# Kernel tuning notes

Measured on AMD Instinct MI355X. Metric: run time of the kernel, lower is better.

The kernel has to match this reference:

```python
import jax, jax.numpy as jnp
import numpy as np

N, E = 20000, 320000
D, DW, DS, NCLS = 512, 300, 16, 13


def setup_inputs() -> dict:
    key = jax.random.key(0)
    ks = jax.random.split(key, 24)
    g = lambda k, s, sc=0.02: (jax.random.normal(k, s, dtype=jnp.float32) * sc)
    inp = {
        'n_f': jax.random.normal(ks[0], (N, D), dtype=jnp.float32),
        'word2vec': jax.random.normal(ks[1], (N, DW), dtype=jnp.float32),
        's_f': jax.random.normal(ks[2], (E, DS), dtype=jnp.float32),
        'src': jax.random.randint(ks[3], (E,), 0, N, dtype=jnp.int32),
        'dst': jax.random.randint(ks[4], (E,), 0, N, dtype=jnp.int32),
        # edge MLPs: G_E_L_S=[2*D+DS, D], G_E_L_S2=[2*DW, D]
        'W_e': g(ks[5], (2 * D + DS, D)), 'b_e': jnp.zeros((D,), jnp.float32),
        'W_el': g(ks[6], (2 * DW, D)), 'b_el': jnp.zeros((D,), jnp.float32),
        # attention MLPs: G_A_L_S=[D,1], G_A_L_S2=[D,1]
        'W_a': g(ks[7], (D, 1)), 'b_a': jnp.zeros((1,), jnp.float32),
        'W_al': g(ks[8], (D, 1)), 'b_al': jnp.zeros((1,), jnp.float32),
        # node MLPs: G_N_L_S=[2*D, D], G_N_L_S2=[2*DW, DW]
        'W_n': g(ks[9], (2 * D, D)), 'b_n': jnp.zeros((D,), jnp.float32),
        'W_nl': g(ks[10], (2 * DW, DW)), 'b_nl': jnp.zeros((DW,), jnp.float32),
        # edge readout: G_ER_L_S=[2*D+2*DW+DS, D, 13], acts ['ReLU','Identity']
        'W_r1': g(ks[11], (2 * D + 2 * DW + DS, D)), 'b_r1': jnp.zeros((D,), jnp.float32),
        'W_r2': g(ks[12], (D, NCLS)), 'b_r2': jnp.zeros((NCLS,), jnp.float32),
    }
    return inp


def _segment_softmax(logits, seg, num_segments):
    m = jax.ops.segment_max(logits, seg, num_segments=num_segments)
    m = jnp.where(jnp.isfinite(m), m, 0.0)
    e = jnp.exp(logits - m[seg])
    s = jax.ops.segment_sum(e, seg, num_segments=num_segments)
    return e / (s[seg] + 1e-9)


def _forward(n_f, word2vec, s_f, W_e, b_e, W_el, b_el, W_a, b_a, W_al, b_al,
             W_n, b_n, W_nl, b_nl, W_r1, b_r1, W_r2, b_r2, src, dst):
    n = n_f.shape[0]
    relu = jax.nn.relu
    # H_H_EdgeApplyModule: e_f = ReLU(MLP([src n_f, s_f, dst n_f]))
    feat = jnp.concatenate([n_f[src], s_f, n_f[dst]], axis=1)            # [E, 2D+DS]
    e_f = relu(feat @ W_e + b_e)                                         # [E, D]
    feat_lang = jnp.concatenate([word2vec[src], word2vec[dst]], axis=1)  # [E, 2DW]
    e_f_lang = relu(feat_lang @ W_el + b_el)                             # [E, D]
    # E_AttentionModule1: LeakyReLU(0.2) attention logits per edge
    a = jax.nn.leaky_relu(e_f @ W_a + b_a, 0.2)[:, 0]
    a_l = jax.nn.leaky_relu(e_f_lang @ W_al + b_al, 0.2)[:, 0]
    # edge-softmax over incoming edges of each destination node
    alpha = _segment_softmax(a, dst, n)
    alpha_l = _segment_softmax(a_l, dst, n)
    # attention-weighted aggregation (scatter-add per dst node)
    z = jax.ops.segment_sum(alpha[:, None] * e_f, dst, num_segments=n)            # [N, D]
    z_l = jax.ops.segment_sum(alpha_l[:, None] * word2vec[src], dst, num_segments=n)  # [N, DW]
    # H_NodeApplyModule: node update with ReLU MLPs
    n_new = relu(jnp.concatenate([n_f, z], axis=1) @ W_n + b_n)          # [N, D]
    w_new = relu(jnp.concatenate([word2vec, z_l], axis=1) @ W_nl + b_nl) # [N, DW]
    # edge readout (G_ER): [src n_f, src w2v, s_f, dst w2v, dst n_f] -> ReLU -> Identity
    r = jnp.concatenate([n_new[src], w_new[src], s_f, w_new[dst], n_new[dst]], axis=1)
    h = relu(r @ W_r1 + b_r1)
    return h @ W_r2 + b_r2                                               # [E, 13]


def reference(n_f, word2vec, s_f, src, dst, W_e, b_e, W_el, b_el, W_a, b_a,
              W_al, b_al, W_n, b_n, W_nl, b_nl, W_r1, b_r1, W_r2, b_r2):
    return _forward(n_f, word2vec, s_f, W_e, b_e, W_el, b_el, W_a, b_a, W_al, b_al,
                    W_n, b_n, W_nl, b_nl, W_r1, b_r1, W_r2, b_r2, src, dst)
```

## Files before the change

kernel.cpp:

```cpp
#include <hip/hip_runtime.h>

typedef unsigned short u16;
typedef unsigned int u32;
typedef __bf16 bf16x8 __attribute__((ext_vector_type(8)));
typedef float f32x4 __attribute__((ext_vector_type(4)));

#define ND 512
#define DWR 300
#define DWP 320
#define NCLS 13

__device__ __forceinline__ float bf2f(u16 u) { return __uint_as_float(((u32)u) << 16); }
__device__ __forceinline__ u16 f2bf(float f) {
    u32 u = __float_as_uint(f);
    u32 r = (u + 0x7FFFu + ((u >> 16) & 1u)) >> 16;
    return (u16)r;
}
__device__ __forceinline__ void ub8(float4 r, float* v) {
    union { float4 f; u16 u[8]; } U; U.f = r;
#pragma unroll
    for (int k = 0; k < 8; ++k) v[k] = bf2f(U.u[k]);
}
__device__ __forceinline__ void ld8f(const u16* p, float* v) { ub8(*(const float4*)p, v); }
__device__ __forceinline__ void ld16(const float* p, float* s) {
    const float4* sp = (const float4*)p;
    float4 s0 = sp[0], s1 = sp[1], s2 = sp[2], s3 = sp[3];
    s[0]=s0.x; s[1]=s0.y; s[2]=s0.z; s[3]=s0.w; s[4]=s1.x; s[5]=s1.y; s[6]=s1.z; s[7]=s1.w;
    s[8]=s2.x; s[9]=s2.y; s[10]=s2.z; s[11]=s2.w; s[12]=s3.x; s[13]=s3.y; s[14]=s3.z; s[15]=s3.w;
}

struct GSeg { const u16* base; const int* idx; int stride; int width; };
struct GSegs { GSeg s[5]; };
struct TSeg { int src_begin; int wreal; int wpad; };
struct TSegs { TSeg t[5]; };

template<int RELU>
__global__ __launch_bounds__(256) void gemm_k(
    int M, int Nout, GSegs segs,
    const u16* __restrict__ BT, int ldb,
    const float* __restrict__ bias, int bias_n,
    u16* __restrict__ outb, int ldo)
{
    __shared__ __align__(16) u16 As[128 * 40];
    __shared__ __align__(16) u16 Bs[128 * 40];
    const int tid = threadIdx.x;

    const int gx = gridDim.x, gy = gridDim.y;
    const int g0 = blockIdx.x + gx * blockIdx.y;
    int xt, yt;
    {
        const int fullg = gx >> 3;
        const int gsz = 8 * gy;
        if (g0 < fullg * gsz) {
            const int grp = g0 / gsz, w = g0 % gsz;
            xt = grp * 8 + (w & 7); yt = w >> 3;
        } else {
            const int remx = gx - fullg * 8;
            const int t = g0 - fullg * gsz;
            xt = fullg * 8 + t % remx; yt = t / remx;
        }
    }
    const int m0 = xt * 128, n0 = yt * 128;

    const int row = tid >> 1, half = tid & 1;
    int mrow = m0 + row; if (mrow >= M) mrow = M - 1;
    const int lane = tid & 63, wid = tid >> 6;
    const int wr = (wid >> 1) * 64, wc = (wid & 1) * 64;
    const int lr = lane & 15, lg = lane >> 4;

    f32x4 acc[4][4];
    for (int fm = 0; fm < 4; fm++)
        for (int fn = 0; fn < 4; fn++)
            acc[fm][fn] = f32x4{0.f, 0.f, 0.f, 0.f};

    const u16* brow = BT + (size_t)(n0 + row) * ldb + half * 16;

    auto do_step = [&](const u16* ga_, const u16* gb_) {
        float4 a0 = *(const float4*)ga_;
        float4 a1 = *(const float4*)(ga_ + 8);
        float4 b0 = *(const float4*)gb_;
        float4 b1 = *(const float4*)(gb_ + 8);
        __syncthreads();
        *(float4*)&As[row * 40 + half * 16]     = a0;
        *(float4*)&As[row * 40 + half * 16 + 8] = a1;
        *(float4*)&Bs[row * 40 + half * 16]     = b0;
        *(float4*)&Bs[row * 40 + half * 16 + 8] = b1;
        __syncthreads();
        bf16x8 af[4], bfv[4];
#pragma unroll
        for (int f = 0; f < 4; f++) {
            af[f]  = *(const bf16x8*)&As[(wr + f * 16 + lr) * 40 + lg * 8];
            bfv[f] = *(const bf16x8*)&Bs[(wc + f * 16 + lr) * 40 + lg * 8];
        }
#pragma unroll
        for (int fm = 0; fm < 4; fm++)
#pragma unroll
            for (int fn = 0; fn < 4; fn++)
                acc[fm][fn] = __builtin_amdgcn_mfma_f32_16x16x32_bf16(af[fm], bfv[fn], acc[fm][fn], 0, 0, 0);
    };

    int k0 = 0;
#pragma unroll
    for (int sI = 0; sI < 5; sI++) {
        const GSeg S = segs.s[sI];
        if (S.width > 0) {
            const int ridx = S.idx ? S.idx[mrow] : mrow;
            const u16* abase = S.base + (size_t)ridx * S.stride + half * 16;
            for (int kk = 0; kk < S.width; kk += 32) {
                do_step(abase + kk, brow + k0 + kk);
            }
            k0 += S.width;
        }
    }

#pragma unroll
    for (int fm = 0; fm < 4; fm++) {
#pragma unroll
        for (int i = 0; i < 4; i++) {
            const int grow = m0 + wr + fm * 16 + lg * 4 + i;
            const bool rok = grow < M;
#pragma unroll
            for (int fn = 0; fn < 4; fn++) {
                const int col = n0 + wc + fn * 16 + lr;
                float v = acc[fm][fn][i];
                v += (col < bias_n) ? bias[col] : 0.f;
                if (RELU) v = fmaxf(v, 0.f);
                if (rok && col < Nout) outb[(size_t)grow * ldo + col] = f2bf(v);
            }
        }
    }
}

__global__ __launch_bounds__(256) void pass1_k(
    const u16* __restrict__ Q, const u16* __restrict__ Lq,
    const float* __restrict__ s_f, const float* __restrict__ wmid,
    const int* __restrict__ psrc, const int* __restrict__ pdst, const int* __restrict__ perm,
    const float* __restrict__ W_a, const float* __restrict__ W_al,
    const float* __restrict__ b_e, const float* __restrict__ b_el,
    const float* __restrict__ b_a, const float* __restrict__ b_al,
    float* __restrict__ aA, float* __restrict__ aL, int E)
{
    __shared__ __align__(16) u16 sfs_bf[128 * 40];
    __shared__ __align__(16) u16 wmidT[512 * 16];
    __shared__ __align__(16) u16 As_v[128 * 40];
    __shared__ __align__(16) u16 As_l[128 * 40];
    __shared__ __align__(16) float sfw[128 * 36];
    __shared__ float bes[512], bels[512];
    __shared__ __align__(16) u16 was[512], wals[512];

    const int tid = threadIdx.x;
    const int e0 = blockIdx.x * 128;

    for (int i = tid; i < 512 * 16; i += 256) {
        const int col = i >> 4, k = i & 15;
        wmidT[i] = f2bf(wmid[k * 512 + col]);
    }
    for (int i = tid; i < 512; i += 256) {
        bes[i] = b_e[i]; bels[i] = b_el[i];
        was[i] = f2bf(W_a[i]); wals[i] = f2bf(W_al[i]);
    }

    const int row = tid >> 1, half = tid & 1;
    const int er = e0 + row;
    const int erc = (er < E) ? er : E - 1;
    {
        const int pe = perm[erc];
        const float4* sp = (const float4*)(s_f + (size_t)pe * 16 + half * 8);
        float4 a = sp[0], b = sp[1];
        union { float4 f; u16 u[8]; } S;
        S.u[0]=f2bf(a.x); S.u[1]=f2bf(a.y); S.u[2]=f2bf(a.z); S.u[3]=f2bf(a.w);
        S.u[4]=f2bf(b.x); S.u[5]=f2bf(b.y); S.u[6]=f2bf(b.z); S.u[7]=f2bf(b.w);
        *(float4*)&sfs_bf[row * 40 + half * 8] = S.f;
        S.f = float4{0.f, 0.f, 0.f, 0.f};
        *(float4*)&sfs_bf[row * 40 + 16 + half * 8] = S.f;
    }

    const int ps = psrc[erc], pd = pdst[erc];
    const u16* q1b = Q + (size_t)ps * 1024;
    const u16* q2b = Q + (size_t)pd * 1024 + 512;
    const u16* l1b = Lq + (size_t)ps * 1024;
    const u16* l2b = Lq + (size_t)pd * 1024 + 512;

    const int lane = tid & 63, wid = tid >> 6;
    const int lr = lane & 15, lg = lane >> 4;
    f32x4 accv[2], accl[2];
    accv[0] = accv[1] = accl[0] = accl[1] = f32x4{0.f, 0.f, 0.f, 0.f};
    union { bf16x8 v; float4 f; } BZ; BZ.f = float4{0.f, 0.f, 0.f, 0.f};

    __syncthreads();

    for (int ch = 0; ch < 16; ++ch) {
        const int k0 = ch * 32 + half * 16;
#pragma unroll
        for (int rt = 0; rt < 2; ++rt) {
            bf16x8 af = *(const bf16x8*)&sfs_bf[((wid * 2 + rt) * 16 + lr) * 40 + lg * 8];
#pragma unroll
            for (int ct = 0; ct < 2; ++ct) {
                const int f = ch * 32 + ct * 16 + lr;
                bf16x8 bf_ = *(const bf16x8*)&wmidT[f * 16 + (lg & 1) * 8];
                f32x4 c = __builtin_amdgcn_mfma_f32_16x16x32_bf16(af, bf_, f32x4{0.f,0.f,0.f,0.f}, 0, 0, 0);
#pragma unroll
                for (int i = 0; i < 4; ++i)
                    sfw[((wid * 2 + rt) * 16 + lg * 4 + i) * 36 + ct * 16 + lr] = c[i];
            }
        }
        __syncthreads();

        float4 rq1a = *(const float4*)(q1b + k0);
        float4 rq1b = *(const float4*)(q1b + k0 + 8);
        float4 rq2a = *(const float4*)(q2b + k0);
        float4 rq2b = *(const float4*)(q2b + k0 + 8);
        float4 rl1a = *(const float4*)(l1b + k0);
        float4 rl1b = *(const float4*)(l1b + k0 + 8);
        float4 rl2a = *(const float4*)(l2b + k0);
        float4 rl2b = *(const float4*)(l2b + k0 + 8);
        float sw[16];
        *(float4*)&sw[0]  = *(const float4*)&sfw[row * 36 + half * 16 + 0];
        *(float4*)&sw[4]  = *(const float4*)&sfw[row * 36 + half * 16 + 4];
        *(float4*)&sw[8]  = *(const float4*)&sfw[row * 36 + half * 16 + 8];
        *(float4*)&sw[12] = *(const float4*)&sfw[row * 36 + half * 16 + 12];

        float uv[16], ul[16], t1[8], t2[8];
        ub8(rq1a, t1); ub8(rq2a, t2);
#pragma unroll
        for (int k = 0; k < 8; ++k) uv[k] = t1[k] + t2[k] + bes[k0 + k] + sw[k];
        ub8(rq1b, t1); ub8(rq2b, t2);
#pragma unroll
        for (int k = 0; k < 8; ++k) uv[8 + k] = t1[k] + t2[k] + bes[k0 + 8 + k] + sw[8 + k];
        ub8(rl1a, t1); ub8(rl2a, t2);
#pragma unroll
        for (int k = 0; k < 8; ++k) ul[k] = t1[k] + t2[k] + bels[k0 + k];
        ub8(rl1b, t1); ub8(rl2b, t2);
#pragma unroll
        for (int k = 0; k < 8; ++k) ul[8 + k] = t1[k] + t2[k] + bels[k0 + 8 + k];

        union { float4 f; u16 u[8]; } Va, Vb, La, Lb;
#pragma unroll
        for (int k = 0; k < 8; ++k) {
            Va.u[k] = f2bf(fmaxf(uv[k], 0.f));
            Vb.u[k] = f2bf(fmaxf(uv[8 + k], 0.f));
            La.u[k] = f2bf(fmaxf(ul[k], 0.f));
            Lb.u[k] = f2bf(fmaxf(ul[8 + k], 0.f));
        }
        *(float4*)&As_v[row * 40 + half * 16]     = Va.f;
        *(float4*)&As_v[row * 40 + half * 16 + 8] = Vb.f;
        *(float4*)&As_l[row * 40 + half * 16]     = La.f;
        *(float4*)&As_l[row * 40 + half * 16 + 8] = Lb.f;
        __syncthreads();

        bf16x8 bv = BZ.v, bl = BZ.v;
        if (lr == 0) {
            bv = *(const bf16x8*)&was[ch * 32 + lg * 8];
            bl = *(const bf16x8*)&wals[ch * 32 + lg * 8];
        }
#pragma unroll
        for (int m = 0; m < 2; ++m) {
            bf16x8 afv = *(const bf16x8*)&As_v[(wid * 32 + m * 16 + lr) * 40 + lg * 8];
            bf16x8 afl = *(const bf16x8*)&As_l[(wid * 32 + m * 16 + lr) * 40 + lg * 8];
            accv[m] = __builtin_amdgcn_mfma_f32_16x16x32_bf16(afv, bv, accv[m], 0, 0, 0);
            accl[m] = __builtin_amdgcn_mfma_f32_16x16x32_bf16(afl, bl, accl[m], 0, 0, 0);
        }
    }

    if (lr == 0) {
        const float ba = b_a[0], bal = b_al[0];
#pragma unroll
        for (int m = 0; m < 2; ++m) {
#pragma unroll
            for (int i = 0; i < 4; ++i) {
                const int e = e0 + wid * 32 + m * 16 + lg * 4 + i;
                if (e < E) {
                    float x = accv[m][i] + ba;
                    aA[e] = x > 0.f ? x : 0.2f * x;
                    float y = accl[m][i] + bal;
                    aL[e] = y > 0.f ? y : 0.2f * y;
                }
            }
        }
    }
}

__global__ __launch_bounds__(256) void softmax_k(
    float* __restrict__ a, float* __restrict__ al,
    const int* __restrict__ offs, int N, int E)
{
    const int node = blockIdx.x * 4 + (threadIdx.x >> 6);
    if (node >= N) return;
    const int lane = threadIdx.x & 63;
    const int e0 = offs[node];
    const int e1 = (node + 1 < N) ? offs[node + 1] : E;
    if (e0 >= e1) return;
    float m = -3.4e38f, ml = -3.4e38f;
    for (int e = e0 + lane; e < e1; e += 64) { m = fmaxf(m, a[e]); ml = fmaxf(ml, al[e]); }
#pragma unroll
    for (int off = 32; off >= 1; off >>= 1) {
        m  = fmaxf(m,  __shfl_xor(m,  off, 64));
        ml = fmaxf(ml, __shfl_xor(ml, off, 64));
    }
    float s = 0.f, sl = 0.f;
    for (int e = e0 + lane; e < e1; e += 64) {
        float v = expf(a[e] - m);   a[e] = v;  s += v;
        float w = expf(al[e] - ml); al[e] = w; sl += w;
    }
#pragma unroll
    for (int off = 32; off >= 1; off >>= 1) {
        s  += __shfl_xor(s,  off, 64);
        sl += __shfl_xor(sl, off, 64);
    }
    const float rs = 1.f / (s + 1e-9f), rsl = 1.f / (sl + 1e-9f);
    for (int e = e0 + lane; e < e1; e += 64) { a[e] *= rs; al[e] *= rsl; }
}

__global__ __launch_bounds__(256) void passz_k(
    const u16* __restrict__ Q, const u16* __restrict__ wv_bf,
    const float* __restrict__ s_f, const float* __restrict__ wmid,
    const int* __restrict__ psrc, const int* __restrict__ perm, const int* __restrict__ offs,
    const float* __restrict__ alpha, const float* __restrict__ alphal,
    const float* __restrict__ b_e,
    u16* __restrict__ z_bf, u16* __restrict__ zl_bf, int N, int E)
{
    __shared__ __align__(16) u16 wmids[16 * 512];
    const int tid = threadIdx.x;
    for (int i = tid; i < 16 * 512; i += 256) wmids[i] = f2bf(wmid[i]);
    __syncthreads();
    const int node = blockIdx.x * 4 + (tid >> 6);
    if (node >= N) return;
    const int lane = tid & 63;
    const int col0 = lane * 8;
    const int colw = (lane < 40) ? col0 : 0;
    const int e0 = offs[node];
    const int e1 = (node + 1 < N) ? offs[node + 1] : E;

    float q2b[8], accz[8], accl[8], t[8];
    ld8f(Q + (size_t)node * 1024 + 512 + col0, q2b);
#pragma unroll
    for (int k = 0; k < 8; ++k) { q2b[k] += b_e[col0 + k]; accz[k] = 0.f; accl[k] = 0.f; }

    if (e0 < e1) {
        int ps0 = psrc[e0], pe0 = perm[e0];
        float4 rq0 = *(const float4*)(Q + (size_t)ps0 * 1024 + col0);
        float4 rw0 = *(const float4*)(wv_bf + (size_t)ps0 * DWP + colw);
        int ps1 = ps0, pe1 = pe0;
        if (e0 + 1 < e1) { ps1 = psrc[e0 + 1]; pe1 = perm[e0 + 1]; }

        for (int e = e0; e < e1; ++e) {
            float4 rq1 = rq0, rw1 = rw0;
            if (e + 1 < e1) {
                rq1 = *(const float4*)(Q + (size_t)ps1 * 1024 + col0);
                rw1 = *(const float4*)(wv_bf + (size_t)ps1 * DWP + colw);
            }
            int ps2 = ps1, pe2 = pe1;
            if (e + 2 < e1) { ps2 = psrc[e + 2]; pe2 = perm[e + 2]; }

            const float alA = alpha[e], alL = alphal[e];
            float sf[16];
            ld16(s_f + (size_t)pe0 * 16, sf);
            float v[8];
            ub8(rq0, t);
#pragma unroll
            for (int k = 0; k < 8; ++k) v[k] = t[k] + q2b[k];
#pragma unroll
            for (int j = 0; j < 16; ++j) {
                union { float4 f; u16 u[8]; } W;
                W.f = *(const float4*)&wmids[j * 512 + col0];
#pragma unroll
                for (int k = 0; k < 8; ++k) v[k] = fmaf(sf[j], bf2f(W.u[k]), v[k]);
            }
#pragma unroll
            for (int k = 0; k < 8; ++k) accz[k] = fmaf(alA, fmaxf(v[k], 0.f), accz[k]);
            ub8(rw0, t);
#pragma unroll
            for (int k = 0; k < 8; ++k) accl[k] = fmaf(alL, t[k], accl[k]);

            rq0 = rq1; rw0 = rw1; ps0 = ps1; pe0 = pe1; ps1 = ps2; pe1 = pe2;
        }
    }
    union { float4 f; u16 u[8]; } O;
#pragma unroll
    for (int k = 0; k < 8; ++k) O.u[k] = f2bf(accz[k]);
    *(float4*)(z_bf + (size_t)node * 512 + col0) = O.f;
    if (lane < 40) {
#pragma unroll
        for (int k = 0; k < 8; ++k) O.u[k] = f2bf(accl[k]);
        *(float4*)(zl_bf + (size_t)node * DWP + col0) = O.f;
    }
}

__global__ __launch_bounds__(256) void pass3_k(
    const u16* __restrict__ P, const float* __restrict__ s_f, const float* __restrict__ wmid2,
    const int* __restrict__ psrc, const int* __restrict__ pdst, const int* __restrict__ perm,
    const float* __restrict__ b_r1, const float* __restrict__ w2, const float* __restrict__ b_r2,
    float* __restrict__ out, int E)
{
    __shared__ __align__(16) u16 As[128 * 40];
    __shared__ __align__(16) u16 sfs_bf[128 * 40];
    __shared__ __align__(16) u16 wmidT[512 * 16];
    __shared__ __align__(16) u16 w2Ts[16 * 520];
    __shared__ __align__(16) float sfw[128 * 36];
    __shared__ float br1s[512];

    const int tid = threadIdx.x;
    const int e0 = blockIdx.x * 128;

    for (int i = tid; i < 512 * 16; i += 256) {
        const int col = i >> 4, k = i & 15;
        wmidT[i] = f2bf(wmid2[k * 512 + col]);
    }
    for (int i = tid; i < 16 * 512; i += 256) {
        const int c = i >> 9, k = i & 511;
        w2Ts[c * 520 + k] = f2bf((c < NCLS) ? w2[k * NCLS + c] : 0.f);
    }
    for (int i = tid; i < 512; i += 256) br1s[i] = b_r1[i];

    const int row = tid >> 1, half = tid & 1;
    const int er = e0 + row;
    const int erc = (er < E) ? er : E - 1;
    {
        const int pe = perm[erc];
        const float4* sp = (const float4*)(s_f + (size_t)pe * 16 + half * 8);
        float4 a = sp[0], b = sp[1];
        union { float4 f; u16 u[8]; } S;
        S.u[0]=f2bf(a.x); S.u[1]=f2bf(a.y); S.u[2]=f2bf(a.z); S.u[3]=f2bf(a.w);
        S.u[4]=f2bf(b.x); S.u[5]=f2bf(b.y); S.u[6]=f2bf(b.z); S.u[7]=f2bf(b.w);
        *(float4*)&sfs_bf[row * 40 + half * 8] = S.f;
        S.f = float4{0.f, 0.f, 0.f, 0.f};
        *(float4*)&sfs_bf[row * 40 + 16 + half * 8] = S.f;
    }

    const int ps = psrc[erc], pd = pdst[erc];
    const u16* p1base = P + (size_t)ps * 1024;
    const u16* p2base = P + (size_t)pd * 1024 + 512;

    const int lane = tid & 63, wid = tid >> 6;
    const int lr = lane & 15, lg = lane >> 4;
    f32x4 acc0 = f32x4{0.f, 0.f, 0.f, 0.f};
    f32x4 acc1 = f32x4{0.f, 0.f, 0.f, 0.f};

    __syncthreads();

    for (int ch = 0; ch < 16; ++ch) {
        const int k0 = ch * 32 + half * 16;
#pragma unroll
        for (int rt = 0; rt < 2; ++rt) {
            bf16x8 af = *(const bf16x8*)&sfs_bf[((wid * 2 + rt) * 16 + lr) * 40 + lg * 8];
#pragma unroll
            for (int ct = 0; ct < 2; ++ct) {
                const int f = ch * 32 + ct * 16 + lr;
                bf16x8 bf_ = *(const bf16x8*)&wmidT[f * 16 + (lg & 1) * 8];
                f32x4 c = __builtin_amdgcn_mfma_f32_16x16x32_bf16(af, bf_, f32x4{0.f,0.f,0.f,0.f}, 0, 0, 0);
#pragma unroll
                for (int i = 0; i < 4; ++i)
                    sfw[((wid * 2 + rt) * 16 + lg * 4 + i) * 36 + ct * 16 + lr] = c[i];
            }
        }
        __syncthreads();

        float4 r1a = *(const float4*)(p1base + k0);
        float4 r1b = *(const float4*)(p1base + k0 + 8);
        float4 r2a = *(const float4*)(p2base + k0);
        float4 r2b = *(const float4*)(p2base + k0 + 8);
        float sw[16];
        *(float4*)&sw[0]  = *(const float4*)&sfw[row * 36 + half * 16 + 0];
        *(float4*)&sw[4]  = *(const float4*)&sfw[row * 36 + half * 16 + 4];
        *(float4*)&sw[8]  = *(const float4*)&sfw[row * 36 + half * 16 + 8];
        *(float4*)&sw[12] = *(const float4*)&sfw[row * 36 + half * 16 + 12];

        float u[16], t1[8], t2[8];
        ub8(r1a, t1); ub8(r2a, t2);
#pragma unroll
        for (int k = 0; k < 8; ++k) u[k] = t1[k] + t2[k] + br1s[k0 + k] + sw[k];
        ub8(r1b, t1); ub8(r2b, t2);
#pragma unroll
        for (int k = 0; k < 8; ++k) u[8 + k] = t1[k] + t2[k] + br1s[k0 + 8 + k] + sw[8 + k];

        union { float4 f; u16 u[8]; } Oa, Ob;
#pragma unroll
        for (int k = 0; k < 8; ++k) {
            Oa.u[k] = f2bf(fmaxf(u[k], 0.f));
            Ob.u[k] = f2bf(fmaxf(u[8 + k], 0.f));
        }
        *(float4*)&As[row * 40 + half * 16]     = Oa.f;
        *(float4*)&As[row * 40 + half * 16 + 8] = Ob.f;
        __syncthreads();

        bf16x8 af0 = *(const bf16x8*)&As[(wid * 32 +      lr) * 40 + lg * 8];
        bf16x8 af1 = *(const bf16x8*)&As[(wid * 32 + 16 + lr) * 40 + lg * 8];
        bf16x8 bfv = *(const bf16x8*)&w2Ts[lr * 520 + ch * 32 + lg * 8];
        acc0 = __builtin_amdgcn_mfma_f32_16x16x32_bf16(af0, bfv, acc0, 0, 0, 0);
        acc1 = __builtin_amdgcn_mfma_f32_16x16x32_bf16(af1, bfv, acc1, 0, 0, 0);
    }

    if (lr < NCLS) {
        const float bc = b_r2[lr];
#pragma unroll
        for (int m = 0; m < 2; ++m) {
            const f32x4 a = m ? acc1 : acc0;
            const int rbase = e0 + wid * 32 + m * 16 + lg * 4;
#pragma unroll
            for (int i = 0; i < 4; ++i) {
                const int ei = rbase + i;
                if (ei < E) out[(size_t)perm[ei] * NCLS + lr] = a[i] + bc;
            }
        }
    }
}

__global__ __launch_bounds__(256) void cvt_bf(const float* __restrict__ src, u16* __restrict__ dst,
                                              int R, int Cs, int Cd)
{
    int id = blockIdx.x * 256 + threadIdx.x;
    if (id >= R * Cd) return;
    int r = id / Cd, c = id % Cd;
    float v = (c < Cs) ? src[(size_t)r * Cs + c] : 0.f;
    dst[id] = f2bf(v);
}

__global__ __launch_bounds__(256) void wtrans(const float* __restrict__ W, int Nw, int Nreal,
                                              int NrowsOut, int ldk, TSegs ts, int nseg,
                                              u16* __restrict__ WT)
{
    int id = blockIdx.x * 256 + threadIdx.x;
    if (id >= NrowsOut * ldk) return;
    int n = id / ldk, kp = id % ldk;
    float v = 0.f;
    if (n < Nreal) {
        int off = 0;
#pragma unroll
        for (int s = 0; s < 5; s++) {
            if (s < nseg) {
                int kl = kp - off;
                if (kl >= 0 && kl < ts.t[s].wpad) {
                    if (kl < ts.t[s].wreal) v = W[(size_t)(ts.t[s].src_begin + kl) * Nw + n];
                }
                off += ts.t[s].wpad;
            }
        }
    }
    WT[id] = f2bf(v);
}

__global__ __launch_bounds__(256) void hist_k(const int* __restrict__ dst, int* __restrict__ deg, int E)
{
    int id = blockIdx.x * 256 + threadIdx.x;
    if (id < E) atomicAdd(&deg[dst[id]], 1);
}

__global__ __launch_bounds__(1024) void scan_k(const int* __restrict__ deg,
                                               int* __restrict__ offs, int* __restrict__ cursor, int N)
{
    __shared__ int ps[1024];
    const int t = threadIdx.x;
    const int per = (N + 1023) >> 10;
    int s = 0;
    for (int j = 0; j < per; j++) { int idx = t * per + j; if (idx < N) s += deg[idx]; }
    ps[t] = s; __syncthreads();
    for (int o = 1; o < 1024; o <<= 1) {
        int v = (t >= o) ? ps[t - o] : 0; __syncthreads();
        ps[t] += v; __syncthreads();
    }
    int run = ps[t] - s;
    for (int j = 0; j < per; j++) {
        int idx = t * per + j;
        if (idx < N) { offs[idx] = run; cursor[idx] = run; run += deg[idx]; }
    }
}

__global__ __launch_bounds__(256) void scat_perm_k(const int* __restrict__ src, const int* __restrict__ dst,
                                                   int* __restrict__ cursor, int* __restrict__ perm,
                                                   int* __restrict__ psrc, int* __restrict__ pdst, int E)
{
    int id = blockIdx.x * 256 + threadIdx.x;
    if (id >= E) return;
    int d = dst[id];
    int pos = atomicAdd(&cursor[d], 1);
    perm[pos] = id; psrc[pos] = src[id]; pdst[pos] = d;
}

__global__ __launch_bounds__(256) void diag_fill(float* out, int n, float v)
{
    int id = blockIdx.x * 256 + threadIdx.x;
    if (id < n) out[id] = v;
}

extern "C" void kernel_launch(void* const* d_in, const int* in_sizes, int n_in,
                              void* d_out, int out_size, void* d_ws, size_t ws_size,
                              hipStream_t stream)
{
    const float* n_f  = (const float*)d_in[0];
    const float* w2v  = (const float*)d_in[1];
    const float* s_f  = (const float*)d_in[2];
    const int*   src  = (const int*)d_in[3];
    const int*   dst  = (const int*)d_in[4];
    const float* W_e  = (const float*)d_in[5];
    const float* b_e  = (const float*)d_in[6];
    const float* W_el = (const float*)d_in[7];
    const float* b_el = (const float*)d_in[8];
    const float* W_a  = (const float*)d_in[9];
    const float* b_a  = (const float*)d_in[10];
    const float* W_al = (const float*)d_in[11];
    const float* b_al = (const float*)d_in[12];
    const float* W_n  = (const float*)d_in[13];
    const float* b_n  = (const float*)d_in[14];
    const float* W_nl = (const float*)d_in[15];
    const float* b_nl = (const float*)d_in[16];
    const float* W_r1 = (const float*)d_in[17];
    const float* b_r1 = (const float*)d_in[18];
    const float* W_r2 = (const float*)d_in[19];
    const float* b_r2 = (const float*)d_in[20];

    const int N = in_sizes[0] / ND;
    const int E = in_sizes[3];
    float* out = (float*)d_out;

    auto g1 = [](long long n) { return dim3((unsigned)((n + 255) / 256)); };

    char* base = (char*)d_ws;
    size_t off = 0;
    auto alloc = [&](size_t bytes) -> void* {
        void* r = base + off;
        off += (bytes + 255) & ~(size_t)255;
        return r;
    };
    u16* nf_bf = (u16*)alloc((size_t)N * ND * 2);
    u16* wv_bf = (u16*)alloc((size_t)N * DWP * 2);
    u16* Q     = (u16*)alloc((size_t)N * 1024 * 2);
    u16* Lq    = (u16*)alloc((size_t)N * 1024 * 2);
    u16* Pt    = (u16*)alloc((size_t)N * 1024 * 2);
    u16* z_bf  = (u16*)alloc((size_t)N * ND * 2);
    u16* zl_bf = (u16*)alloc((size_t)N * DWP * 2);
    u16* nn_bf = (u16*)alloc((size_t)N * ND * 2);
    u16* wn_bf = (u16*)alloc((size_t)N * DWP * 2);
    u16* QT    = (u16*)alloc((size_t)1024 * 512 * 2);
    u16* LT    = (u16*)alloc((size_t)1024 * 320 * 2);
    u16* WnT   = (u16*)alloc((size_t)512 * 1024 * 2);
    u16* WnlT  = (u16*)alloc((size_t)384 * 640 * 2);
    u16* PrT   = (u16*)alloc((size_t)1024 * 832 * 2);
    float* aAs = (float*)alloc((size_t)E * 4);
    float* aLs = (float*)alloc((size_t)E * 4);
    int* deg    = (int*)alloc((size_t)N * 4);
    int* offs   = (int*)alloc((size_t)N * 4);
    int* cursor = (int*)alloc((size_t)N * 4);
    int* perm   = (int*)alloc((size_t)E * 4);
    int* psrc   = (int*)alloc((size_t)E * 4);
    int* pdst   = (int*)alloc((size_t)E * 4);

    if (off > ws_size) {
        diag_fill<<<g1(out_size), 256, 0, stream>>>(out, out_size, 2.0e6f);
        return;
    }

    hipMemsetAsync(deg, 0, (size_t)N * 4, stream);

    hist_k<<<g1(E), 256, 0, stream>>>(dst, deg, E);
    scan_k<<<dim3(1), 1024, 0, stream>>>(deg, offs, cursor, N);
    scat_perm_k<<<g1(E), 256, 0, stream>>>(src, dst, cursor, perm, psrc, pdst, E);

    cvt_bf<<<g1((long long)N * ND), 256, 0, stream>>>(n_f, nf_bf, N, ND, ND);
    cvt_bf<<<g1((long long)N * DWP), 256, 0, stream>>>(w2v, wv_bf, N, DWR, DWP);

    { TSegs t{}; t.t[0] = {0,512,512};
      wtrans<<<g1(512 * 512), 256, 0, stream>>>(W_e, 512, 512, 512, 512, t, 1, QT); }
    { TSegs t{}; t.t[0] = {528,512,512};
      wtrans<<<g1(512 * 512), 256, 0, stream>>>(W_e, 512, 512, 512, 512, t, 1, QT + 512 * 512); }
    { TSegs t{}; t.t[0] = {0,300,320};
      wtrans<<<g1(512 * 320), 256, 0, stream>>>(W_el, 512, 512, 512, 320, t, 1, LT); }
    { TSegs t{}; t.t[0] = {300,300,320};
      wtrans<<<g1(512 * 320), 256, 0, stream>>>(W_el, 512, 512, 512, 320, t, 1, LT + 512 * 320); }
    { TSegs t{}; t.t[0] = {0,512,512}; t.t[1] = {512,512,512};
      wtrans<<<g1(512 * 1024), 256, 0, stream>>>(W_n, 512, 512, 512, 1024, t, 2, WnT); }
    { TSegs t{}; t.t[0] = {0,300,320}; t.t[1] = {300,300,320};
      wtrans<<<g1(384 * 640), 256, 0, stream>>>(W_nl, 300, 300, 384, 640, t, 2, WnlT); }
    { TSegs t{}; t.t[0] = {0,512,512}; t.t[1] = {512,300,320};
      wtrans<<<g1(512 * 832), 256, 0, stream>>>(W_r1, 512, 512, 512, 832, t, 2, PrT); }
    { TSegs t{}; t.t[0] = {1128,512,512}; t.t[1] = {828,300,320};
      wtrans<<<g1(512 * 832), 256, 0, stream>>>(W_r1, 512, 512, 512, 832, t, 2, PrT + 512 * 832); }

    const int gmx = (N + 127) / 128;
    const dim3 gnode((N + 3) / 4);

    { GSegs s{}; s.s[0] = {nf_bf, nullptr, ND, 512};
      gemm_k<0><<<dim3(gmx, 8), 256, 0, stream>>>(N, 1024, s, QT, 512, nullptr, 0, Q, 1024); }
    { GSegs s{}; s.s[0] = {wv_bf, nullptr, DWP, 320};
      gemm_k<0><<<dim3(gmx, 8), 256, 0, stream>>>(N, 1024, s, LT, 320, nullptr, 0, Lq, 1024); }

    pass1_k<<<dim3((E + 127) / 128), 256, 0, stream>>>(Q, Lq, s_f, W_e + 512 * 512,
                                                       psrc, pdst, perm, W_a, W_al,
                                                       b_e, b_el, b_a, b_al, aAs, aLs, E);
    softmax_k<<<gnode, 256, 0, stream>>>(aAs, aLs, offs, N, E);

    passz_k<<<gnode, 256, 0, stream>>>(Q, wv_bf, s_f, W_e + 512 * 512, psrc, perm, offs,
                                       aAs, aLs, b_e, z_bf, zl_bf, N, E);

    { GSegs s{}; s.s[0] = {nf_bf, nullptr, ND, 512}; s.s[1] = {z_bf, nullptr, ND, 512};
      gemm_k<1><<<dim3(gmx, 4), 256, 0, stream>>>(N, 512, s, WnT, 1024, b_n, 512, nn_bf, 512); }
    { GSegs s{}; s.s[0] = {wv_bf, nullptr, DWP, 320}; s.s[1] = {zl_bf, nullptr, DWP, 320};
      gemm_k<1><<<dim3(gmx, 3), 256, 0, stream>>>(N, 320, s, WnlT, 640, b_nl, 300, wn_bf, DWP); }

    { GSegs s{}; s.s[0] = {nn_bf, nullptr, ND, 512}; s.s[1] = {wn_bf, nullptr, DWP, 320};
      gemm_k<0><<<dim3(gmx, 8), 256, 0, stream>>>(N, 1024, s, PrT, 832, nullptr, 0, Pt, 1024); }

    pass3_k<<<dim3((E + 127) / 128), 256, 0, stream>>>(Pt, s_f, W_r1 + 812 * 512,
                                                       psrc, pdst, perm, b_r1, W_r2, b_r2, out, E);

    hipError_t e = hipGetLastError();
    if (e != hipSuccess) {
        diag_fill<<<g1(out_size), 256, 0, stream>>>(out, out_size, 1.0e6f + (float)(int)e);
    }
}
```

Measured before the change: 939.7 us.

## Restructure edge aggregation as edge-parallel MFMA kernel with atomics and XCD swizzle

The per-node z aggregation, which recomputed the s_f·W_mid projection with scalar FMAs, is replaced by an edge-parallel kernel. That kernel computes the projection with bf16 MFMA on 128-edge tiles and scatters alpha-weighted ReLU outputs into an fp32 buffer using segmented runs followed by atomicAdd. The z_l aggregation moves to its own lightweight per-node kernel, and a memset plus a conversion kernel are added to produce bf16 z. Edge kernels also remap block indices to keep contiguous edge tiles on the same XCD for cache locality. The trade-offs are extra launches, atomic contention, and reusing the Lq buffer as fp32 scratch.

```diff
diff --git a/kernel.cpp b/kernel.cpp
--- a/kernel.cpp
+++ b/kernel.cpp
@@ -22,11 +22,10 @@
     for (int k = 0; k < 8; ++k) v[k] = bf2f(U.u[k]);
 }
 __device__ __forceinline__ void ld8f(const u16* p, float* v) { ub8(*(const float4*)p, v); }
-__device__ __forceinline__ void ld16(const float* p, float* s) {
-    const float4* sp = (const float4*)p;
-    float4 s0 = sp[0], s1 = sp[1], s2 = sp[2], s3 = sp[3];
-    s[0]=s0.x; s[1]=s0.y; s[2]=s0.z; s[3]=s0.w; s[4]=s1.x; s[5]=s1.y; s[6]=s1.z; s[7]=s1.w;
-    s[8]=s2.x; s[9]=s2.y; s[10]=s2.z; s[11]=s2.w; s[12]=s3.x; s[13]=s3.y; s[14]=s3.z; s[15]=s3.w;
+__device__ __forceinline__ int xcd_swz(int b, int gx) {
+    const int q = gx >> 3, r = gx & 7;
+    const int x = b & 7, o = b >> 3;
+    return (x < r ? x * (q + 1) : r * (q + 1) + (x - r) * q) + o;
 }
 
 struct GSeg { const u16* base; const int* idx; int stride; int width; };
@@ -149,7 +148,7 @@
     __shared__ __align__(16) u16 was[512], wals[512];
 
     const int tid = threadIdx.x;
-    const int e0 = blockIdx.x * 128;
+    const int e0 = xcd_swz(blockIdx.x, gridDim.x) * 128;
 
     for (int i = tid; i < 512 * 16; i += 256) {
         const int col = i >> 4, k = i & 15;
@@ -311,78 +310,138 @@
     for (int e = e0 + lane; e < e1; e += 64) { a[e] *= rs; al[e] *= rsl; }
 }
 
-__global__ __launch_bounds__(256) void passz_k(
-    const u16* __restrict__ Q, const u16* __restrict__ wv_bf,
-    const float* __restrict__ s_f, const float* __restrict__ wmid,
-    const int* __restrict__ psrc, const int* __restrict__ perm, const int* __restrict__ offs,
-    const float* __restrict__ alpha, const float* __restrict__ alphal,
-    const float* __restrict__ b_e,
-    u16* __restrict__ z_bf, u16* __restrict__ zl_bf, int N, int E)
-{
-    __shared__ __align__(16) u16 wmids[16 * 512];
+__global__ __launch_bounds__(256) void passzt_k(
+    const u16* __restrict__ Q, const float* __restrict__ s_f, const float* __restrict__ wmid,
+    const int* __restrict__ psrc, const int* __restrict__ pdst, const int* __restrict__ perm,
+    const float* __restrict__ alpha, const float* __restrict__ b_e,
+    float* __restrict__ z, int E)
+{
+    __shared__ __align__(16) u16 sfs_bf[128 * 40];
+    __shared__ __align__(16) u16 wmidT[512 * 16];
+    __shared__ __align__(16) float sfw[128 * 36];
+    __shared__ float bes[512];
+    __shared__ int pd[128];
+    __shared__ float alf[128];
+
     const int tid = threadIdx.x;
-    for (int i = tid; i < 16 * 512; i += 256) wmids[i] = f2bf(wmid[i]);
+    const int e0 = xcd_swz(blockIdx.x, gridDim.x) * 128;
+
+    for (int i = tid; i < 512 * 16; i += 256) {
+        const int col = i >> 4, k = i & 15;
+        wmidT[i] = f2bf(wmid[k * 512 + col]);
+    }
+    for (int i = tid; i < 512; i += 256) bes[i] = b_e[i];
+
+    const int row = tid >> 1, half = tid & 1;
+    const int er = e0 + row;
+    const int erc = (er < E) ? er : E - 1;
+    {
+        const int pe = perm[erc];
+        const float4* sp = (const float4*)(s_f + (size_t)pe * 16 + half * 8);
+        float4 a = sp[0], b = sp[1];
+        union { float4 f; u16 u[8]; } S;
+        S.u[0]=f2bf(a.x); S.u[1]=f2bf(a.y); S.u[2]=f2bf(a.z); S.u[3]=f2bf(a.w);
+        S.u[4]=f2bf(b.x); S.u[5]=f2bf(b.y); S.u[6]=f2bf(b.z); S.u[7]=f2bf(b.w);
+        *(float4*)&sfs_bf[row * 40 + half * 8] = S.f;
+        S.f = float4{0.f, 0.f, 0.f, 0.f};
+        *(float4*)&sfs_bf[row * 40 + 16 + half * 8] = S.f;
+    }
+    if (half == 0) {
+        pd[row] = pdst[erc];
+        alf[row] = (er < E) ? alpha[er] : 0.f;
+    }
+
+    const int ps = psrc[erc], pdn = pdst[erc];
+    const u16* q1b = Q + (size_t)ps * 1024;
+    const u16* q2b = Q + (size_t)pdn * 1024 + 512;
+
+    const int lane = tid & 63, wid = tid >> 6;
+    const int lr = lane & 15, lg = lane >> 4;
+
     __syncthreads();
-    const int node = blockIdx.x * 4 + (tid >> 6);
+
+    for (int ch = 0; ch < 16; ++ch) {
+        const int k0 = ch * 32 + half * 16;
+#pragma unroll
+        for (int rt = 0; rt < 2; ++rt) {
+            bf16x8 af = *(const bf16x8*)&sfs_bf[((wid * 2 + rt) * 16 + lr) * 40 + lg * 8];
+#pragma unroll
+            for (int ct = 0; ct < 2; ++ct) {
+                const int f = ch * 32 + ct * 16 + lr;
+                bf16x8 bf_ = *(const bf16x8*)&wmidT[f * 16 + (lg & 1) * 8];
+                f32x4 c = __builtin_amdgcn_mfma_f32_16x16x32_bf16(af, bf_, f32x4{0.f,0.f,0.f,0.f}, 0, 0, 0);
+#pragma unroll
+                for (int i = 0; i < 4; ++i)
+                    sfw[((wid * 2 + rt) * 16 + lg * 4 + i) * 36 + ct * 16 + lr] = c[i];
+            }
+        }
+        __syncthreads();
+
+        {
+            float4 r1a = *(const float4*)(q1b + k0);
+            float4 r1b = *(const float4*)(q1b + k0 + 8);
+            float4 r2a = *(const float4*)(q2b + k0);
+            float4 r2b = *(const float4*)(q2b + k0 + 8);
+            float sw[16];
+            *(float4*)&sw[0]  = *(const float4*)&sfw[row * 36 + half * 16 + 0];
+            *(float4*)&sw[4]  = *(const float4*)&sfw[row * 36 + half * 16 + 4];
+            *(float4*)&sw[8]  = *(const float4*)&sfw[row * 36 + half * 16 + 8];
+            *(float4*)&sw[12] = *(const float4*)&sfw[row * 36 + half * 16 + 12];
+            float u[16], t1[8], t2[8];
+            ub8(r1a, t1); ub8(r2a, t2);
+#pragma unroll
+            for (int k = 0; k < 8; ++k) u[k] = t1[k] + t2[k] + bes[k0 + k] + sw[k];
+            ub8(r1b, t1); ub8(r2b, t2);
+#pragma unroll
+            for (int k = 0; k < 8; ++k) u[8 + k] = t1[k] + t2[k] + bes[k0 + 8 + k] + sw[8 + k];
+            const float av = alf[row];
+#pragma unroll
+            for (int k = 0; k < 16; ++k) u[k] = av * fmaxf(u[k], 0.f);
+            *(float4*)&sfw[row * 36 + half * 16 + 0]  = *(float4*)&u[0];
+            *(float4*)&sfw[row * 36 + half * 16 + 4]  = *(float4*)&u[4];
+            *(float4*)&sfw[row * 36 + half * 16 + 8]  = *(float4*)&u[8];
+            *(float4*)&sfw[row * 36 + half * 16 + 12] = *(float4*)&u[12];
+        }
+        __syncthreads();
+
+        {
+            const int c = tid & 31, g = tid >> 5;
+            const int r0 = g * 16;
+            float run = 0.f; int cur = pd[r0];
+            for (int r = r0; r < r0 + 16; ++r) {
+                run += sfw[r * 36 + c];
+                const int nxt = (r < r0 + 15) ? pd[r + 1] : -1;
+                if (nxt != cur) {
+                    atomicAdd(&z[(size_t)cur * 512 + ch * 32 + c], run);
+                    run = 0.f; cur = nxt;
+                }
+            }
+        }
+        __syncthreads();
+    }
+}
+
+__global__ __launch_bounds__(256) void agg_zl_k(
+    const u16* __restrict__ wv_bf, const float* __restrict__ alphal,
+    const int* __restrict__ psrc, const int* __restrict__ offs,
+    u16* __restrict__ zl_bf, int N, int E)
+{
+    const int node = blockIdx.x * 4 + (threadIdx.x >> 6);
     if (node >= N) return;
-    const int lane = tid & 63;
-    const int col0 = lane * 8;
-    const int colw = (lane < 40) ? col0 : 0;
+    const int lane = threadIdx.x & 63;
     const int e0 = offs[node];
     const int e1 = (node + 1 < N) ? offs[node + 1] : E;
-
-    float q2b[8], accz[8], accl[8], t[8];
-    ld8f(Q + (size_t)node * 1024 + 512 + col0, q2b);
-#pragma unroll
-    for (int k = 0; k < 8; ++k) { q2b[k] += b_e[col0 + k]; accz[k] = 0.f; accl[k] = 0.f; }
-
-    if (e0 < e1) {
-        int ps0 = psrc[e0], pe0 = perm[e0];
-        float4 rq0 = *(const float4*)(Q + (size_t)ps0 * 1024 + col0);
-        float4 rw0 = *(const float4*)(wv_bf + (size_t)ps0 * DWP + colw);
-        int ps1 = ps0, pe1 = pe0;
-        if (e0 + 1 < e1) { ps1 = psrc[e0 + 1]; pe1 = perm[e0 + 1]; }
-
-        for (int e = e0; e < e1; ++e) {
-            float4 rq1 = rq0, rw1 = rw0;
-            if (e + 1 < e1) {
-                rq1 = *(const float4*)(Q + (size_t)ps1 * 1024 + col0);
-                rw1 = *(const float4*)(wv_bf + (size_t)ps1 * DWP + colw);
-            }
-            int ps2 = ps1, pe2 = pe1;
-            if (e + 2 < e1) { ps2 = psrc[e + 2]; pe2 = perm[e + 2]; }
-
-            const float alA = alpha[e], alL = alphal[e];
-            float sf[16];
-            ld16(s_f + (size_t)pe0 * 16, sf);
-            float v[8];
-            ub8(rq0, t);
-#pragma unroll
-            for (int k = 0; k < 8; ++k) v[k] = t[k] + q2b[k];
-#pragma unroll
-            for (int j = 0; j < 16; ++j) {
-                union { float4 f; u16 u[8]; } W;
-                W.f = *(const float4*)&wmids[j * 512 + col0];
-#pragma unroll
-                for (int k = 0; k < 8; ++k) v[k] = fmaf(sf[j], bf2f(W.u[k]), v[k]);
-            }
-#pragma unroll
-            for (int k = 0; k < 8; ++k) accz[k] = fmaf(alA, fmaxf(v[k], 0.f), accz[k]);
-            ub8(rw0, t);
-#pragma unroll
-            for (int k = 0; k < 8; ++k) accl[k] = fmaf(alL, t[k], accl[k]);
-
-            rq0 = rq1; rw0 = rw1; ps0 = ps1; pe0 = pe1; ps1 = ps2; pe1 = pe2;
-        }
-    }
-    union { float4 f; u16 u[8]; } O;
-#pragma unroll
-    for (int k = 0; k < 8; ++k) O.u[k] = f2bf(accz[k]);
-    *(float4*)(z_bf + (size_t)node * 512 + col0) = O.f;
-    if (lane < 40) {
-#pragma unroll
-        for (int k = 0; k < 8; ++k) O.u[k] = f2bf(accl[k]);
-        *(float4*)(zl_bf + (size_t)node * DWP + col0) = O.f;
+    float acc[5] = {0.f, 0.f, 0.f, 0.f, 0.f};
+    for (int e = e0; e < e1; ++e) {
+        const float al = alphal[e];
+        const u16* wr = wv_bf + (size_t)psrc[e] * DWP;
+#pragma unroll
+        for (int j = 0; j < 5; ++j) acc[j] += al * bf2f(wr[lane + 64 * j]);
+    }
+#pragma unroll
+    for (int j = 0; j < 5; ++j) {
+        const int c = lane + 64 * j;
+        zl_bf[(size_t)node * DWP + c] = f2bf(c < DWR ? acc[j] : 0.f);
     }
 }
 
@@ -400,7 +459,7 @@
     __shared__ float br1s[512];
 
     const int tid = threadIdx.x;
-    const int e0 = blockIdx.x * 128;
+    const int e0 = xcd_swz(blockIdx.x, gridDim.x) * 128;
 
     for (int i = tid; i < 512 * 16; i += 256) {
         const int col = i >> 4, k = i & 15;
@@ -643,6 +702,7 @@
     int* perm   = (int*)alloc((size_t)E * 4);
     int* psrc   = (int*)alloc((size_t)E * 4);
     int* pdst   = (int*)alloc((size_t)E * 4);
+    float* zf = (float*)Lq;
 
     if (off > ws_size) {
         diag_fill<<<g1(out_size), 256, 0, stream>>>(out, out_size, 2.0e6f);
@@ -677,19 +737,23 @@
 
     const int gmx = (N + 127) / 128;
     const dim3 gnode((N + 3) / 4);
+    const dim3 gedge((E + 127) / 128);
 
     { GSegs s{}; s.s[0] = {nf_bf, nullptr, ND, 512};
       gemm_k<0><<<dim3(gmx, 8), 256, 0, stream>>>(N, 1024, s, QT, 512, nullptr, 0, Q, 1024); }
     { GSegs s{}; s.s[0] = {wv_bf, nullptr, DWP, 320};
       gemm_k<0><<<dim3(gmx, 8), 256, 0, stream>>>(N, 1024, s, LT, 320, nullptr, 0, Lq, 1024); }
 
-    pass1_k<<<dim3((E + 127) / 128), 256, 0, stream>>>(Q, Lq, s_f, W_e + 512 * 512,
-                                                       psrc, pdst, perm, W_a, W_al,
-                                                       b_e, b_el, b_a, b_al, aAs, aLs, E);
+    pass1_k<<<gedge, 256, 0, stream>>>(Q, Lq, s_f, W_e + 512 * 512,
+                                       psrc, pdst, perm, W_a, W_al,
+                                       b_e, b_el, b_a, b_al, aAs, aLs, E);
     softmax_k<<<gnode, 256, 0, stream>>>(aAs, aLs, offs, N, E);
 
-    passz_k<<<gnode, 256, 0, stream>>>(Q, wv_bf, s_f, W_e + 512 * 512, psrc, perm, offs,
-                                       aAs, aLs, b_e, z_bf, zl_bf, N, E);
+    hipMemsetAsync(zf, 0, (size_t)N * 512 * 4, stream);
+    passzt_k<<<gedge, 256, 0, stream>>>(Q, s_f, W_e + 512 * 512, psrc, pdst, perm,
+                                        aAs, b_e, zf, E);
+    agg_zl_k<<<gnode, 256, 0, stream>>>(wv_bf, aLs, psrc, offs, zl_bf, N, E);
+    cvt_bf<<<g1((long long)N * ND), 256, 0, stream>>>(zf, z_bf, N, ND, ND);
 
     { GSegs s{}; s.s[0] = {nf_bf, nullptr, ND, 512}; s.s[1] = {z_bf, nullptr, ND, 512};
       gemm_k<1><<<dim3(gmx, 4), 256, 0, stream>>>(N, 512, s, WnT, 1024, b_n, 512, nn_bf, 512); }
@@ -699,8 +763,8 @@
     { GSegs s{}; s.s[0] = {nn_bf, nullptr, ND, 512}; s.s[1] = {wn_bf, nullptr, DWP, 320};
       gemm_k<0><<<dim3(gmx, 8), 256, 0, stream>>>(N, 1024, s, PrT, 832, nullptr, 0, Pt, 1024); }
 
-    pass3_k<<<dim3((E + 127) / 128), 256, 0, stream>>>(Pt, s_f, W_r1 + 812 * 512,
-                                                       psrc, pdst, perm, b_r1, W_r2, b_r2, out, E);
+    pass3_k<<<gedge, 256, 0, stream>>>(Pt, s_f, W_r1 + 812 * 512,
+                                       psrc, pdst, perm, b_r1, W_r2, b_r2, out, E);
 
     hipError_t e = hipGetLastError();
     if (e != hipSuccess) {
```

After: 977.6 us. 4.0% more time.
